# Optimization experiments

Hardware: AMD Instinct MI355X
Metric: run time of the kernel (lower is better)

Reference implementation:

```python
import jax, jax.numpy as jnp
import numpy as np

N_HEADS, N_LEVELS, N_POINTS, D_MODEL = 8, 4, 4, 256
HEAD_DIM = D_MODEL // N_HEADS
SHAPES = [(96, 96), (48, 48), (24, 24), (12, 12)]


def setup_inputs() -> dict:
    key = jax.random.key(0)
    ks = jax.random.split(key, 9)
    shapes_np = np.asarray(SHAPES, dtype=np.int32)
    lengths = shapes_np[:, 0] * shapes_np[:, 1]
    Len = int(lengths.sum())  # 12240
    B = 1
    level_start = np.concatenate([[0], np.cumsum(lengths)[:-1]]).astype(np.int32)
    return {
        "query": jax.random.normal(ks[0], (B, Len, D_MODEL), jnp.float32),
        "reference_points": jax.random.uniform(ks[1], (B, Len, 2), jnp.float32),
        "input_flatten": jax.random.normal(ks[2], (B, Len, D_MODEL), jnp.float32),
        "spatial_shapes": jnp.asarray(shapes_np),
        "level_start_index": jnp.asarray(level_start),
        "W_off": jax.random.normal(ks[3], (D_MODEL, N_HEADS * N_LEVELS * N_POINTS * 2), jnp.float32) * 0.01,
        "b_off": jax.random.normal(ks[4], (N_HEADS * N_LEVELS * N_POINTS * 2,), jnp.float32) * 0.01,
        "W_attn": jax.random.normal(ks[5], (D_MODEL, N_HEADS * N_LEVELS * N_POINTS), jnp.float32) * 0.02,
        "b_attn": jnp.zeros((N_HEADS * N_LEVELS * N_POINTS,), jnp.float32),
        "W_out": jax.random.normal(ks[6], (D_MODEL, D_MODEL), jnp.float32) * 0.02,
        "b_out": jnp.zeros((D_MODEL,), jnp.float32),
    }


def _bilinear_gather(feat, x, y, H, W):
    """feat: [B,nH,H*W,D]; x,y: [B,nH,S] pixel coords. Zero padding, align_corners=False."""
    x0 = jnp.floor(x)
    y0 = jnp.floor(y)
    wx1 = x - x0
    wy1 = y - y0
    wx0 = 1.0 - wx1
    wy0 = 1.0 - wy1
    x0i = x0.astype(jnp.int32)
    y0i = y0.astype(jnp.int32)

    def corner(ix, iy):
        valid = (ix >= 0) & (ix < W) & (iy >= 0) & (iy < H)
        idx = jnp.clip(iy, 0, H - 1) * W + jnp.clip(ix, 0, W - 1)
        g = jnp.take_along_axis(feat, idx[..., None], axis=2)  # [B,nH,S,D]
        return g * valid[..., None].astype(feat.dtype)

    return (corner(x0i, y0i) * (wx0 * wy0)[..., None]
            + corner(x0i + 1, y0i) * (wx1 * wy0)[..., None]
            + corner(x0i, y0i + 1) * (wx0 * wy1)[..., None]
            + corner(x0i + 1, y0i + 1) * (wx1 * wy1)[..., None])


def _ms_deform_core(value, shapes_np, loc, attn):
    """value: [B,Len_in,nH,D]; loc: [B,LQ,nH,nL,nP,2]; attn: [B,LQ,nH,nL,nP]."""
    B, LQ = loc.shape[0], loc.shape[1]
    lengths = [int(h) * int(w) for h, w in shapes_np]
    starts = np.concatenate([[0], np.cumsum(lengths)])
    out = jnp.zeros((B, N_HEADS, LQ, HEAD_DIM), value.dtype)
    for lvl, (H, W) in enumerate(shapes_np):
        H, W = int(H), int(W)
        feat = value[:, starts[lvl]:starts[lvl + 1]].transpose(0, 2, 1, 3)  # [B,nH,HW,D]
        l = loc[:, :, :, lvl]  # [B,LQ,nH,nP,2]
        x = (l[..., 0] * W - 0.5).transpose(0, 2, 1, 3).reshape(B, N_HEADS, LQ * N_POINTS)
        y = (l[..., 1] * H - 0.5).transpose(0, 2, 1, 3).reshape(B, N_HEADS, LQ * N_POINTS)
        samp = _bilinear_gather(feat, x, y, H, W).reshape(B, N_HEADS, LQ, N_POINTS, HEAD_DIM)
        w = attn[:, :, :, lvl].transpose(0, 2, 1, 3)  # [B,nH,LQ,nP]
        out = out + (samp * w[..., None]).sum(axis=3)
    return out.transpose(0, 2, 1, 3).reshape(B, LQ, N_HEADS * HEAD_DIM)


def reference(query, reference_points, input_flatten, spatial_shapes, level_start_index,
              W_off, b_off, W_attn, b_attn, W_out, b_out):
    B, LQ, C = query.shape
    shapes_np = np.asarray(spatial_shapes)  # static per-level (H,W)
    off = (query @ W_off + b_off).reshape(B, LQ, N_HEADS, N_LEVELS, N_POINTS, 2)
    attn = jax.nn.softmax((query @ W_attn + b_attn).reshape(B, LQ, N_HEADS, N_LEVELS * N_POINTS), axis=-1)
    attn = attn.reshape(B, LQ, N_HEADS, N_LEVELS, N_POINTS)
    # offset_normalizer = (W, H) per level
    norm = jnp.asarray(np.stack([shapes_np[:, 1], shapes_np[:, 0]], -1), dtype=query.dtype)
    loc = reference_points[:, :, None, None, None, :] + off / norm[None, None, None, :, None, :]
    value = input_flatten.reshape(B, -1, N_HEADS, HEAD_DIM)
    out = _ms_deform_core(value, shapes_np, loc, attn)
    return out @ W_out + b_out
```

## Files before the change

### kernel.cpp

```cpp
#include <hip/hip_runtime.h>
#include <hip/hip_bf16.h>
#include <math.h>

constexpr int D_MODEL  = 256;
constexpr int N_HEADS  = 8;

typedef __attribute__((ext_vector_type(8))) short bf16x8;
typedef __attribute__((ext_vector_type(4))) float f32x4;
typedef __attribute__((ext_vector_type(2))) float f32x2;

__device__ __forceinline__ void gld_lds16(const void* gsrc, void* ldst) {
    __builtin_amdgcn_global_load_lds(
        (const __attribute__((address_space(1))) unsigned int*)gsrc,
        (__attribute__((address_space(3))) unsigned int*)ldst, 16, 0, 0);
}

__global__ __launch_bounds__(256) void convert_kernel(
    const float* __restrict__ q,
    const float* __restrict__ Woff,
    const float* __restrict__ Wattn,
    const float* __restrict__ Wout,
    const float* __restrict__ value,
    __hip_bfloat16* __restrict__ qbf,
    __hip_bfloat16* __restrict__ wt,
    __hip_bfloat16* __restrict__ vt,
    int M, int Lv)
{
    int t = blockIdx.x * 256 + threadIdx.x;
    int nq4 = M * 64;
    if (t < nq4) {
        float4 v = reinterpret_cast<const float4*>(q)[t];
        union { __hip_bfloat16 h[4]; ushort4 u; } cv;
        cv.h[0] = __float2bfloat16(v.x);
        cv.h[1] = __float2bfloat16(v.y);
        cv.h[2] = __float2bfloat16(v.z);
        cv.h[3] = __float2bfloat16(v.w);
        reinterpret_cast<ushort4*>(qbf)[t] = cv.u;
        return;
    }
    int t2 = t - nq4;
    if (t2 < 640 * 256) {
        int c = t2 >> 8, k = t2 & 255;
        float val = (c < 256) ? Woff[k * 256 + c]
                  : (c < 384) ? Wattn[k * 128 + (c - 256)]
                              : Wout[k * 256 + (c - 384)];
        wt[c * 256 + k] = __float2bfloat16(val);
        return;
    }
    int t3 = t2 - 640 * 256;
    if (t3 < Lv * 64) {
        int pix = t3 >> 6;
        int c4  = (t3 & 63) * 4;
        int h   = c4 >> 5, d = c4 & 31;
        float4 v = reinterpret_cast<const float4*>(value)[t3];
        union { __hip_bfloat16 h4[4]; ushort4 u; } cv;
        cv.h4[0] = __float2bfloat16(v.x);
        cv.h4[1] = __float2bfloat16(v.y);
        cv.h4[2] = __float2bfloat16(v.z);
        cv.h4[3] = __float2bfloat16(v.w);
        *reinterpret_cast<ushort4*>(vt + (size_t)h * Lv * 32 + (size_t)pix * 32 + d) = cv.u;
    }
}

template <int EPI>
__global__ __launch_bounds__(256) void gemm_mfma(
    const __hip_bfloat16* __restrict__ Abf,
    const __hip_bfloat16* __restrict__ Wt,
    int wrow0,
    const float* __restrict__ ba,
    const float* __restrict__ bb,
    const float* __restrict__ refpts,
    float* __restrict__ out0,
    float* __restrict__ out1,
    int M)
{
    __shared__ __align__(16) char smem[128 * 68 * 4];
    char*  A_lds = smem;
    char*  B_lds = smem + 16384;
    float* C_lds = (float*)smem;

    const int tid = threadIdx.x;
    const int w = tid >> 6, l = tid & 63;
    const int m0 = blockIdx.y * 128;
    const int n0 = blockIdx.x * 64;

    const char* Asrc = (const char*)Abf;
    const char* Wsrc = (const char*)(Wt + (size_t)(wrow0 + n0) * 256);

    f32x4 acc[2][4] = {};

    const int lr8 = l >> 3, l7 = l & 7;

    for (int k0 = 0; k0 < 512; k0 += 128) {
#pragma unroll
        for (int i = 0; i < 4; ++i) {
            int chunk = (w << 2) + i;
            int row = (chunk << 3) + lr8;
            int m = m0 + row; m = m < M ? m : (M - 1);
            gld_lds16(Asrc + (size_t)m * 512 + k0 + ((l7 ^ (row & 7)) << 4),
                      A_lds + (chunk << 10));
        }
#pragma unroll
        for (int i = 0; i < 2; ++i) {
            int chunk = (w << 1) + i;
            int row = (chunk << 3) + lr8;
            gld_lds16(Wsrc + (size_t)row * 512 + k0 + ((l7 ^ (row & 7)) << 4),
                      B_lds + (chunk << 10));
        }
        __syncthreads();

#pragma unroll
        for (int kk = 0; kk < 2; ++kk) {
            bf16x8 av[2], bv[4];
#pragma unroll
            for (int mf = 0; mf < 2; ++mf) {
                int arow = (w << 5) + (mf << 4) + (l & 15);
                int acb = ((kk << 6) + ((l >> 4) << 4)) ^ ((arow & 7) << 4);
                av[mf] = *(const bf16x8*)(A_lds + arow * 128 + acb);
            }
#pragma unroll
            for (int nf = 0; nf < 4; ++nf) {
                int brow = (nf << 4) + (l & 15);
                int bcb = ((kk << 6) + ((l >> 4) << 4)) ^ ((brow & 7) << 4);
                bv[nf] = *(const bf16x8*)(B_lds + brow * 128 + bcb);
            }
#pragma unroll
            for (int mf = 0; mf < 2; ++mf)
#pragma unroll
                for (int nf = 0; nf < 4; ++nf)
                    acc[mf][nf] = __builtin_amdgcn_mfma_f32_16x16x32_bf16(
                        av[mf], bv[nf], acc[mf][nf], 0, 0, 0);
        }
        __syncthreads();
    }

#pragma unroll
    for (int mf = 0; mf < 2; ++mf)
#pragma unroll
        for (int nf = 0; nf < 4; ++nf) {
            int col = (nf << 4) + (l & 15);
            int rbase = (w << 5) + (mf << 4) + ((l >> 4) << 2);
#pragma unroll
            for (int j = 0; j < 4; ++j)
                C_lds[(rbase + j) * 68 + col] = acc[mf][nf][j];
        }
    __syncthreads();

    if (EPI == 0 || n0 < 256) {
#pragma unroll
        for (int r2 = 0; r2 < 2; ++r2) {
            int row = (r2 << 6) + (tid >> 2);
            int q = m0 + row;
            if (q >= M) continue;
            float rx = 0.f, ry = 0.f;
            if (EPI == 1) { rx = refpts[q * 2]; ry = refpts[q * 2 + 1]; }
#pragma unroll
            for (int g = 0; g < 4; ++g) {
                int col = ((tid & 3) << 4) + (g << 2);
                float4 v  = *(float4*)&C_lds[row * 68 + col];
                float4 b4 = *(const float4*)&ba[n0 + col];
                if (EPI == 0) {
                    v.x += b4.x; v.y += b4.y; v.z += b4.z; v.w += b4.w;
                } else {
                    int c = n0 + col;
                    float rn = 1.0f / (float)(96 >> ((c >> 3) & 3));
                    v.x = rx + (v.x + b4.x) * rn;
                    v.y = ry + (v.y + b4.y) * rn;
                    v.z = rx + (v.z + b4.z) * rn;
                    v.w = ry + (v.w + b4.w) * rn;
                }
                *(float4*)&out0[(size_t)q * 256 + n0 + col] = v;
            }
        }
    } else {
        for (int u = tid; u < 512; u += 256) {
            int row = u >> 2, hh = u & 3;
            int q = m0 + row;
            if (q >= M) continue;
            int cg = (n0 - 256) + (hh << 4);
            float s[16];
            float mx = -1e30f;
#pragma unroll
            for (int i = 0; i < 16; ++i) {
                s[i] = C_lds[row * 68 + (hh << 4) + i] + bb[cg + i];
                mx = fmaxf(mx, s[i]);
            }
            float sum = 0.f;
#pragma unroll
            for (int i = 0; i < 16; ++i) { s[i] = __expf(s[i] - mx); sum += s[i]; }
            float inv = 1.0f / sum;
#pragma unroll
            for (int g = 0; g < 4; ++g) {
                float4 v = make_float4(s[g*4]*inv, s[g*4+1]*inv, s[g*4+2]*inv, s[g*4+3]*inv);
                *(float4*)&out1[(size_t)q * 128 + cg + (g << 2)] = v;
            }
        }
    }
}

template <int IMM>
__device__ __forceinline__ float swzf(float v) {
    return __int_as_float(__builtin_amdgcn_ds_swizzle(__float_as_int(v), IMM));
}
template <int IMM>
__device__ __forceinline__ int swzi(int v) {
    return __builtin_amdgcn_ds_swizzle(v, IMM);
}

__device__ __forceinline__ f32x2 bf2(unsigned v) {
    f32x2 r;
    r.x = __uint_as_float(v << 16);
    r.y = __uint_as_float(v & 0xffff0000u);
    return r;
}
__device__ __forceinline__ unsigned packbf(float lo, float hi) {
    __hip_bfloat16 a = __float2bfloat16(lo), b = __float2bfloat16(hi);
    return (unsigned)*(unsigned short*)&a | ((unsigned)*(unsigned short*)&b << 16);
}

template <int P>
__device__ __forceinline__ void do_point4(
    const float wv[4][4], const int ov[4][4], const char* planeB,
    f32x2& a0, f32x2& a1, f32x2& a2, f32x2& a3)
{
    constexpr int S   = P & 3;
    constexpr int IMM = ((P >> 2) << 5) | 0x1C;

    float w00 = swzf<IMM>(wv[S][0]);
    float w10 = swzf<IMM>(wv[S][1]);
    float w01 = swzf<IMM>(wv[S][2]);
    float w11 = swzf<IMM>(wv[S][3]);
    int o00 = swzi<IMM>(ov[S][0]);
    int o10 = swzi<IMM>(ov[S][1]);
    int o01 = swzi<IMM>(ov[S][2]);
    int o11 = swzi<IMM>(ov[S][3]);

    uint4 u0 = *(const uint4*)(planeB + o00);
    uint4 u1 = *(const uint4*)(planeB + o10);
    uint4 u2 = *(const uint4*)(planeB + o01);
    uint4 u3 = *(const uint4*)(planeB + o11);

    { f32x2 w2 = {w00, w00};
      a0 += bf2(u0.x) * w2; a1 += bf2(u0.y) * w2;
      a2 += bf2(u0.z) * w2; a3 += bf2(u0.w) * w2; }
    { f32x2 w2 = {w10, w10};
      a0 += bf2(u1.x) * w2; a1 += bf2(u1.y) * w2;
      a2 += bf2(u1.z) * w2; a3 += bf2(u1.w) * w2; }
    { f32x2 w2 = {w01, w01};
      a0 += bf2(u2.x) * w2; a1 += bf2(u2.y) * w2;
      a2 += bf2(u2.z) * w2; a3 += bf2(u2.w) * w2; }
    { f32x2 w2 = {w11, w11};
      a0 += bf2(u3.x) * w2; a1 += bf2(u3.y) * w2;
      a2 += bf2(u3.z) * w2; a3 += bf2(u3.w) * w2; }
}

__global__ __launch_bounds__(256, 4) void sample_kernel(
    const float* __restrict__ loc,
    const float* __restrict__ attn,
    const __hip_bfloat16* __restrict__ vt,
    __hip_bfloat16* __restrict__ core,
    int M, int Lv)
{
    const int h  = blockIdx.x & 7;
    const int q0 = (blockIdx.x >> 3) << 6;
    const int u_ = threadIdx.x >> 2;
    const int j  = threadIdx.x & 3;
    const int q  = q0 + u_;
    if (q >= M) return;

    const int Wl    = 96 >> j;
    const int start = 12288 - (12288 >> (2 * j));
    const float fW  = (float)Wl;

    const float4* lq4 = (const float4*)(loc + (size_t)q * 256 + h * 32 + j * 8);
    float4 pa = lq4[0];
    float4 pb = lq4[1];
    float4 aw = *(const float4*)(attn + (size_t)q * 128 + h * 16 + j * 4);

    const float lxs[4] = {pa.x, pa.z, pb.x, pb.z};
    const float lys[4] = {pa.y, pa.w, pb.y, pb.w};
    const float aws[4] = {aw.x, aw.y, aw.z, aw.w};

    float wv[4][4]; int ov[4][4];
#pragma unroll
    for (int s = 0; s < 4; ++s) {
        float x = lxs[s] * fW - 0.5f;
        float y = lys[s] * fW - 0.5f;
        float wgt = aws[s];

        float xf = floorf(x), yf = floorf(y);
        float wx1 = x - xf, wy1 = y - yf;
        float wx0 = 1.f - wx1, wy0 = 1.f - wy1;
        int ix = (int)xf, iy = (int)yf;

        float wxv0 = ((unsigned)ix       < (unsigned)Wl) ? wx0 : 0.f;
        float wxv1 = ((unsigned)(ix + 1) < (unsigned)Wl) ? wx1 : 0.f;
        float wyv0 = (((unsigned)iy       < (unsigned)Wl) ? wy0 : 0.f) * wgt;
        float wyv1 = (((unsigned)(iy + 1) < (unsigned)Wl) ? wy1 : 0.f) * wgt;

        int ix0 = min(max(ix,     0), Wl - 1);
        int ix1 = min(max(ix + 1, 0), Wl - 1);
        int iy0 = min(max(iy,     0), Wl - 1);
        int iy1 = min(max(iy + 1, 0), Wl - 1);

        int r0 = start + iy0 * Wl, r1 = start + iy1 * Wl;
        wv[s][0] = wxv0 * wyv0;  ov[s][0] = (r0 + ix0) << 6;
        wv[s][1] = wxv1 * wyv0;  ov[s][1] = (r0 + ix1) << 6;
        wv[s][2] = wxv0 * wyv1;  ov[s][2] = (r1 + ix0) << 6;
        wv[s][3] = wxv1 * wyv1;  ov[s][3] = (r1 + ix1) << 6;
    }

    const char* planeB = (const char*)vt + (size_t)h * Lv * 64 + j * 16;
    f32x2 a0 = {0.f, 0.f}, a1 = a0, a2 = a0, a3 = a0;

    do_point4< 0>(wv, ov, planeB, a0, a1, a2, a3);
    do_point4< 1>(wv, ov, planeB, a0, a1, a2, a3);
    do_point4< 2>(wv, ov, planeB, a0, a1, a2, a3);
    do_point4< 3>(wv, ov, planeB, a0, a1, a2, a3);
    do_point4< 4>(wv, ov, planeB, a0, a1, a2, a3);
    do_point4< 5>(wv, ov, planeB, a0, a1, a2, a3);
    do_point4< 6>(wv, ov, planeB, a0, a1, a2, a3);
    do_point4< 7>(wv, ov, planeB, a0, a1, a2, a3);
    do_point4< 8>(wv, ov, planeB, a0, a1, a2, a3);
    do_point4< 9>(wv, ov, planeB, a0, a1, a2, a3);
    do_point4<10>(wv, ov, planeB, a0, a1, a2, a3);
    do_point4<11>(wv, ov, planeB, a0, a1, a2, a3);
    do_point4<12>(wv, ov, planeB, a0, a1, a2, a3);
    do_point4<13>(wv, ov, planeB, a0, a1, a2, a3);
    do_point4<14>(wv, ov, planeB, a0, a1, a2, a3);
    do_point4<15>(wv, ov, planeB, a0, a1, a2, a3);

    uint4 st;
    st.x = packbf(a0.x, a0.y);
    st.y = packbf(a1.x, a1.y);
    st.z = packbf(a2.x, a2.y);
    st.w = packbf(a3.x, a3.y);
    *(uint4*)((char*)core + ((size_t)q * 256 + h * 32 + j * 8) * 2) = st;
}

extern "C" void kernel_launch(void* const* d_in, const int* in_sizes, int n_in,
                              void* d_out, int out_size, void* d_ws, size_t ws_size,
                              hipStream_t stream)
{
    const float* query  = (const float*)d_in[0];
    const float* refp   = (const float*)d_in[1];
    const float* value  = (const float*)d_in[2];
    const float* W_off  = (const float*)d_in[5];
    const float* b_off  = (const float*)d_in[6];
    const float* W_attn = (const float*)d_in[7];
    const float* b_attn = (const float*)d_in[8];
    const float* W_out  = (const float*)d_in[9];
    const float* b_out  = (const float*)d_in[10];
    float* out = (float*)d_out;

    const int M  = in_sizes[0] / D_MODEL;
    const int Lv = in_sizes[2] / D_MODEL;

    float* loc  = (float*)d_ws;
    float* attn = loc + (size_t)M * 256;
    __hip_bfloat16* qbf = (__hip_bfloat16*)(attn + (size_t)M * 128);
    __hip_bfloat16* wt  = qbf + (size_t)M * 256;
    __hip_bfloat16* vt  = wt + 640 * 256;
    __hip_bfloat16* core = qbf;

    dim3 blk(256);
    const int mblocks = (M + 127) / 128;

    int convthreads = M * 64 + 640 * 256 + Lv * 64;
    hipLaunchKernelGGL(convert_kernel, dim3((convthreads + 255) / 256), blk, 0, stream,
                       query, W_off, W_attn, W_out, value, qbf, wt, vt, M, Lv);

    hipLaunchKernelGGL((gemm_mfma<1>), dim3(6, mblocks), blk, 0, stream,
                       qbf, wt, 0, b_off, b_attn, refp, loc, attn, M);

    const int qchunks = (M + 63) / 64;
    hipLaunchKernelGGL(sample_kernel, dim3(qchunks * 8), blk, 0, stream,
                       loc, attn, vt, core, M, Lv);

    hipLaunchKernelGGL((gemm_mfma<0>), dim3(4, mblocks), blk, 0, stream,
                       core, wt, 384, b_out, nullptr, nullptr, out, nullptr, M);
}
```

Before: 60.54 us.

## Widen GEMM N-tile to 128 and pack sampling weights/offsets for fewer swizzles

The MFMA GEMM now computes 128 output columns per block instead of 64, halving the grid in x and reusing each A tile across twice as many columns, with the epilogue done in two 64-column halves through the same LDS buffer. The sampling kernel packs the four bilinear corner weights into bf16 pairs and the corner indices into 16-bit pairs, halving the ds_swizzle cross-lane broadcasts per point. Costs are higher accumulator register pressure and fewer blocks in the GEMMs. The weights also lose precision by going through bf16, and the packing assumes row indices fit in 16 bits.

```diff
diff --git a/kernel.cpp b/kernel.cpp
--- a/kernel.cpp
+++ b/kernel.cpp
@@ -82,12 +82,12 @@
     const int tid = threadIdx.x;
     const int w = tid >> 6, l = tid & 63;
     const int m0 = blockIdx.y * 128;
-    const int n0 = blockIdx.x * 64;
+    const int n0 = blockIdx.x * 128;
 
     const char* Asrc = (const char*)Abf;
     const char* Wsrc = (const char*)(Wt + (size_t)(wrow0 + n0) * 256);
 
-    f32x4 acc[2][4] = {};
+    f32x4 acc[2][8] = {};
 
     const int lr8 = l >> 3, l7 = l & 7;
 
@@ -101,8 +101,8 @@
                       A_lds + (chunk << 10));
         }
 #pragma unroll
-        for (int i = 0; i < 2; ++i) {
-            int chunk = (w << 1) + i;
+        for (int i = 0; i < 4; ++i) {
+            int chunk = (w << 2) + i;
             int row = (chunk << 3) + lr8;
             gld_lds16(Wsrc + (size_t)row * 512 + k0 + ((l7 ^ (row & 7)) << 4),
                       B_lds + (chunk << 10));
@@ -111,7 +111,7 @@
 
 #pragma unroll
         for (int kk = 0; kk < 2; ++kk) {
-            bf16x8 av[2], bv[4];
+            bf16x8 av[2], bv[8];
 #pragma unroll
             for (int mf = 0; mf < 2; ++mf) {
                 int arow = (w << 5) + (mf << 4) + (l & 15);
@@ -119,7 +119,7 @@
                 av[mf] = *(const bf16x8*)(A_lds + arow * 128 + acb);
             }
 #pragma unroll
-            for (int nf = 0; nf < 4; ++nf) {
+            for (int nf = 0; nf < 8; ++nf) {
                 int brow = (nf << 4) + (l & 15);
                 int bcb = ((kk << 6) + ((l >> 4) << 4)) ^ ((brow & 7) << 4);
                 bv[nf] = *(const bf16x8*)(B_lds + brow * 128 + bcb);
@@ -127,7 +127,7 @@
 #pragma unroll
             for (int mf = 0; mf < 2; ++mf)
 #pragma unroll
-                for (int nf = 0; nf < 4; ++nf)
+                for (int nf = 0; nf < 8; ++nf)
                     acc[mf][nf] = __builtin_amdgcn_mfma_f32_16x16x32_bf16(
                         av[mf], bv[nf], acc[mf][nf], 0, 0, 0);
         }
@@ -135,73 +135,75 @@
     }
 
 #pragma unroll
-    for (int mf = 0; mf < 2; ++mf)
-#pragma unroll
-        for (int nf = 0; nf < 4; ++nf) {
-            int col = (nf << 4) + (l & 15);
-            int rbase = (w << 5) + (mf << 4) + ((l >> 4) << 2);
-#pragma unroll
-            for (int j = 0; j < 4; ++j)
-                C_lds[(rbase + j) * 68 + col] = acc[mf][nf][j];
+    for (int hf = 0; hf < 2; ++hf) {
+#pragma unroll
+        for (int mf = 0; mf < 2; ++mf)
+#pragma unroll
+            for (int nf2 = 0; nf2 < 4; ++nf2) {
+                int nf = (hf << 2) + nf2;
+                int col = (nf2 << 4) + (l & 15);
+                int rbase = (w << 5) + (mf << 4) + ((l >> 4) << 2);
+#pragma unroll
+                for (int j = 0; j < 4; ++j)
+                    C_lds[(rbase + j) * 68 + col] = acc[mf][nf][j];
+            }
+        __syncthreads();
+
+        if (EPI == 0 || n0 < 256) {
+#pragma unroll
+            for (int r2 = 0; r2 < 2; ++r2) {
+                int row = (r2 << 6) + (tid >> 2);
+                int q = m0 + row;
+                if (q < M) {
+                    float rx = 0.f, ry = 0.f;
+                    if (EPI == 1) { rx = refpts[q * 2]; ry = refpts[q * 2 + 1]; }
+#pragma unroll
+                    for (int g = 0; g < 4; ++g) {
+                        int col = ((tid & 3) << 4) + (g << 2);
+                        int c = n0 + (hf << 6) + col;
+                        float4 v  = *(float4*)&C_lds[row * 68 + col];
+                        float4 b4 = *(const float4*)&ba[c];
+                        if (EPI == 0) {
+                            v.x += b4.x; v.y += b4.y; v.z += b4.z; v.w += b4.w;
+                        } else {
+                            float rn = 1.0f / (float)(96 >> ((c >> 3) & 3));
+                            v.x = rx + (v.x + b4.x) * rn;
+                            v.y = ry + (v.y + b4.y) * rn;
+                            v.z = rx + (v.z + b4.z) * rn;
+                            v.w = ry + (v.w + b4.w) * rn;
+                        }
+                        *(float4*)&out0[(size_t)q * 256 + c] = v;
+                    }
+                }
+            }
+        } else {
+            for (int u = tid; u < 512; u += 256) {
+                int row = u >> 2, hh = u & 3;
+                int q = m0 + row;
+                if (q >= M) continue;
+                int cg = (hf << 6) + (hh << 4);
+                float s[16];
+                float mx = -1e30f;
+#pragma unroll
+                for (int i = 0; i < 16; ++i) {
+                    s[i] = C_lds[row * 68 + (hh << 4) + i] + bb[cg + i];
+                    mx = fmaxf(mx, s[i]);
+                }
+                float sum = 0.f;
+#pragma unroll
+                for (int i = 0; i < 16; ++i) { s[i] = __expf(s[i] - mx); sum += s[i]; }
+                float inv = 1.0f / sum;
+#pragma unroll
+                for (int g = 0; g < 4; ++g) {
+                    float4 v = make_float4(s[g*4]*inv, s[g*4+1]*inv, s[g*4+2]*inv, s[g*4+3]*inv);
+                    *(float4*)&out1[(size_t)q * 128 + cg + (g << 2)] = v;
+                }
+            }
         }
-    __syncthreads();
-
-    if (EPI == 0 || n0 < 256) {
-#pragma unroll
-        for (int r2 = 0; r2 < 2; ++r2) {
-            int row = (r2 << 6) + (tid >> 2);
-            int q = m0 + row;
-            if (q >= M) continue;
-            float rx = 0.f, ry = 0.f;
-            if (EPI == 1) { rx = refpts[q * 2]; ry = refpts[q * 2 + 1]; }
-#pragma unroll
-            for (int g = 0; g < 4; ++g) {
-                int col = ((tid & 3) << 4) + (g << 2);
-                float4 v  = *(float4*)&C_lds[row * 68 + col];
-                float4 b4 = *(const float4*)&ba[n0 + col];
-                if (EPI == 0) {
-                    v.x += b4.x; v.y += b4.y; v.z += b4.z; v.w += b4.w;
-                } else {
-                    int c = n0 + col;
-                    float rn = 1.0f / (float)(96 >> ((c >> 3) & 3));
-                    v.x = rx + (v.x + b4.x) * rn;
-                    v.y = ry + (v.y + b4.y) * rn;
-                    v.z = rx + (v.z + b4.z) * rn;
-                    v.w = ry + (v.w + b4.w) * rn;
-                }
-                *(float4*)&out0[(size_t)q * 256 + n0 + col] = v;
-            }
-        }
-    } else {
-        for (int u = tid; u < 512; u += 256) {
-            int row = u >> 2, hh = u & 3;
-            int q = m0 + row;
-            if (q >= M) continue;
-            int cg = (n0 - 256) + (hh << 4);
-            float s[16];
-            float mx = -1e30f;
-#pragma unroll
-            for (int i = 0; i < 16; ++i) {
-                s[i] = C_lds[row * 68 + (hh << 4) + i] + bb[cg + i];
-                mx = fmaxf(mx, s[i]);
-            }
-            float sum = 0.f;
-#pragma unroll
-            for (int i = 0; i < 16; ++i) { s[i] = __expf(s[i] - mx); sum += s[i]; }
-            float inv = 1.0f / sum;
-#pragma unroll
-            for (int g = 0; g < 4; ++g) {
-                float4 v = make_float4(s[g*4]*inv, s[g*4+1]*inv, s[g*4+2]*inv, s[g*4+3]*inv);
-                *(float4*)&out1[(size_t)q * 128 + cg + (g << 2)] = v;
-            }
-        }
-    }
-}
-
-template <int IMM>
-__device__ __forceinline__ float swzf(float v) {
-    return __int_as_float(__builtin_amdgcn_ds_swizzle(__float_as_int(v), IMM));
-}
+        __syncthreads();
+    }
+}
+
 template <int IMM>
 __device__ __forceinline__ int swzi(int v) {
     return __builtin_amdgcn_ds_swizzle(v, IMM);
@@ -220,36 +222,39 @@
 
 template <int P>
 __device__ __forceinline__ void do_point4(
-    const float wv[4][4], const int ov[4][4], const char* planeB,
+    const unsigned wp[4][2], const int op[4][2], const char* planeB,
     f32x2& a0, f32x2& a1, f32x2& a2, f32x2& a3)
 {
     constexpr int S   = P & 3;
     constexpr int IMM = ((P >> 2) << 5) | 0x1C;
 
-    float w00 = swzf<IMM>(wv[S][0]);
-    float w10 = swzf<IMM>(wv[S][1]);
-    float w01 = swzf<IMM>(wv[S][2]);
-    float w11 = swzf<IMM>(wv[S][3]);
-    int o00 = swzi<IMM>(ov[S][0]);
-    int o10 = swzi<IMM>(ov[S][1]);
-    int o01 = swzi<IMM>(ov[S][2]);
-    int o11 = swzi<IMM>(ov[S][3]);
+    unsigned wA = (unsigned)swzi<IMM>((int)wp[S][0]);
+    unsigned wB = (unsigned)swzi<IMM>((int)wp[S][1]);
+    unsigned oA = (unsigned)swzi<IMM>(op[S][0]);
+    unsigned oB = (unsigned)swzi<IMM>(op[S][1]);
+
+    f32x2 wlo = bf2(wA);
+    f32x2 whi = bf2(wB);
+    int o00 = (int)((oA & 0xffffu) << 6);
+    int o10 = (int)((oA >> 16) << 6);
+    int o01 = (int)((oB & 0xffffu) << 6);
+    int o11 = (int)((oB >> 16) << 6);
 
     uint4 u0 = *(const uint4*)(planeB + o00);
     uint4 u1 = *(const uint4*)(planeB + o10);
     uint4 u2 = *(const uint4*)(planeB + o01);
     uint4 u3 = *(const uint4*)(planeB + o11);
 
-    { f32x2 w2 = {w00, w00};
+    { f32x2 w2 = {wlo.x, wlo.x};
       a0 += bf2(u0.x) * w2; a1 += bf2(u0.y) * w2;
       a2 += bf2(u0.z) * w2; a3 += bf2(u0.w) * w2; }
-    { f32x2 w2 = {w10, w10};
+    { f32x2 w2 = {wlo.y, wlo.y};
       a0 += bf2(u1.x) * w2; a1 += bf2(u1.y) * w2;
       a2 += bf2(u1.z) * w2; a3 += bf2(u1.w) * w2; }
-    { f32x2 w2 = {w01, w01};
+    { f32x2 w2 = {whi.x, whi.x};
       a0 += bf2(u2.x) * w2; a1 += bf2(u2.y) * w2;
       a2 += bf2(u2.z) * w2; a3 += bf2(u2.w) * w2; }
-    { f32x2 w2 = {w11, w11};
+    { f32x2 w2 = {whi.y, whi.y};
       a0 += bf2(u3.x) * w2; a1 += bf2(u3.y) * w2;
       a2 += bf2(u3.z) * w2; a3 += bf2(u3.w) * w2; }
 }
@@ -281,7 +286,7 @@
     const float lys[4] = {pa.y, pa.w, pb.y, pb.w};
     const float aws[4] = {aw.x, aw.y, aw.z, aw.w};
 
-    float wv[4][4]; int ov[4][4];
+    unsigned wp[4][2]; int op[4][2];
 #pragma unroll
     for (int s = 0; s < 4; ++s) {
         float x = lxs[s] * fW - 0.5f;
@@ -304,31 +309,31 @@
         int iy1 = min(max(iy + 1, 0), Wl - 1);
 
         int r0 = start + iy0 * Wl, r1 = start + iy1 * Wl;
-        wv[s][0] = wxv0 * wyv0;  ov[s][0] = (r0 + ix0) << 6;
-        wv[s][1] = wxv1 * wyv0;  ov[s][1] = (r0 + ix1) << 6;
-        wv[s][2] = wxv0 * wyv1;  ov[s][2] = (r1 + ix0) << 6;
-        wv[s][3] = wxv1 * wyv1;  ov[s][3] = (r1 + ix1) << 6;
+        wp[s][0] = packbf(wxv0 * wyv0, wxv1 * wyv0);
+        wp[s][1] = packbf(wxv0 * wyv1, wxv1 * wyv1);
+        op[s][0] = (r0 + ix0) | ((r0 + ix1) << 16);
+        op[s][1] = (r1 + ix0) | ((r1 + ix1) << 16);
     }
 
     const char* planeB = (const char*)vt + (size_t)h * Lv * 64 + j * 16;
     f32x2 a0 = {0.f, 0.f}, a1 = a0, a2 = a0, a3 = a0;
 
-    do_point4< 0>(wv, ov, planeB, a0, a1, a2, a3);
-    do_point4< 1>(wv, ov, planeB, a0, a1, a2, a3);
-    do_point4< 2>(wv, ov, planeB, a0, a1, a2, a3);
-    do_point4< 3>(wv, ov, planeB, a0, a1, a2, a3);
-    do_point4< 4>(wv, ov, planeB, a0, a1, a2, a3);
-    do_point4< 5>(wv, ov, planeB, a0, a1, a2, a3);
-    do_point4< 6>(wv, ov, planeB, a0, a1, a2, a3);
-    do_point4< 7>(wv, ov, planeB, a0, a1, a2, a3);
-    do_point4< 8>(wv, ov, planeB, a0, a1, a2, a3);
-    do_point4< 9>(wv, ov, planeB, a0, a1, a2, a3);
-    do_point4<10>(wv, ov, planeB, a0, a1, a2, a3);
-    do_point4<11>(wv, ov, planeB, a0, a1, a2, a3);
-    do_point4<12>(wv, ov, planeB, a0, a1, a2, a3);
-    do_point4<13>(wv, ov, planeB, a0, a1, a2, a3);
-    do_point4<14>(wv, ov, planeB, a0, a1, a2, a3);
-    do_point4<15>(wv, ov, planeB, a0, a1, a2, a3);
+    do_point4< 0>(wp, op, planeB, a0, a1, a2, a3);
+    do_point4< 1>(wp, op, planeB, a0, a1, a2, a3);
+    do_point4< 2>(wp, op, planeB, a0, a1, a2, a3);
+    do_point4< 3>(wp, op, planeB, a0, a1, a2, a3);
+    do_point4< 4>(wp, op, planeB, a0, a1, a2, a3);
+    do_point4< 5>(wp, op, planeB, a0, a1, a2, a3);
+    do_point4< 6>(wp, op, planeB, a0, a1, a2, a3);
+    do_point4< 7>(wp, op, planeB, a0, a1, a2, a3);
+    do_point4< 8>(wp, op, planeB, a0, a1, a2, a3);
+    do_point4< 9>(wp, op, planeB, a0, a1, a2, a3);
+    do_point4<10>(wp, op, planeB, a0, a1, a2, a3);
+    do_point4<11>(wp, op, planeB, a0, a1, a2, a3);
+    do_point4<12>(wp, op, planeB, a0, a1, a2, a3);
+    do_point4<13>(wp, op, planeB, a0, a1, a2, a3);
+    do_point4<14>(wp, op, planeB, a0, a1, a2, a3);
+    do_point4<15>(wp, op, planeB, a0, a1, a2, a3);
 
     uint4 st;
     st.x = packbf(a0.x, a0.y);
@@ -370,13 +375,13 @@
     hipLaunchKernelGGL(convert_kernel, dim3((convthreads + 255) / 256), blk, 0, stream,
                        query, W_off, W_attn, W_out, value, qbf, wt, vt, M, Lv);
 
-    hipLaunchKernelGGL((gemm_mfma<1>), dim3(6, mblocks), blk, 0, stream,
+    hipLaunchKernelGGL((gemm_mfma<1>), dim3(3, mblocks), blk, 0, stream,
                        qbf, wt, 0, b_off, b_attn, refp, loc, attn, M);
 
     const int qchunks = (M + 63) / 64;
     hipLaunchKernelGGL(sample_kernel, dim3(qchunks * 8), blk, 0, stream,
                        loc, attn, vt, core, M, Lv);
 
-    hipLaunchKernelGGL((gemm_mfma<0>), dim3(4, mblocks), blk, 0, stream,
+    hipLaunchKernelGGL((gemm_mfma<0>), dim3(2, mblocks), blk, 0, stream,
                        core, wt, 384, b_out, nullptr, nullptr, out, nullptr, M);
 }
```

Result: no change. 61.13 us (+1.0%).
